# Kernel optimization log

Hardware: AMD Instinct MI355X
Metric: run time of the kernel (lower is better)

Reference implementation:

```python
import jax, jax.numpy as jnp
import numpy as np

EMBED_SIZE = 768
HEAD_SIZE = 64
B, T = 4, 2048


def setup_inputs() -> dict:
    key = jax.random.key(0)
    kx, kk, kq, kv = jax.random.split(key, 4)
    x = jax.random.normal(kx, (B, T, EMBED_SIZE), dtype=jnp.float32)
    # torch Linear(E, H, bias=False): weight [H, E]; stored here as [E, H] for x @ W
    s = 1.0 / np.sqrt(EMBED_SIZE)
    Wk = jax.random.uniform(kk, (EMBED_SIZE, HEAD_SIZE), jnp.float32, -s, s)
    Wq = jax.random.uniform(kq, (EMBED_SIZE, HEAD_SIZE), jnp.float32, -s, s)
    Wv = jax.random.uniform(kv, (EMBED_SIZE, HEAD_SIZE), jnp.float32, -s, s)
    return {"x": x, "Wk": Wk, "Wq": Wq, "Wv": Wv}


def reference(x, Wk, Wq, Wv):
    Bx, Tx, E = x.shape
    k = x @ Wk  # [B, T, H]
    q = x @ Wq
    v = x @ Wv
    w = jnp.einsum("bth,bsh->bts", q, k)  # [B, T, T]
    causal = jnp.tril(jnp.ones((Tx, Tx), dtype=bool))
    # Faithful to source: mask to -inf FIRST, then scale by sqrt(embed_size)
    w = jnp.where(causal, w, -jnp.inf)
    w = w / jnp.sqrt(jnp.asarray(E, dtype=x.dtype))
    w = jax.nn.softmax(w, axis=-1)
    # dropout: eval mode / identity for the correctness baseline
    return jnp.einsum("bts,bsh->bth", w, v)
```

## Files before the change

### kernel.cpp

```cpp
#include <hip/hip_runtime.h>
#include <hip/hip_bf16.h>


typedef __attribute__((ext_vector_type(8))) short short8;
typedef __attribute__((ext_vector_type(4))) float f32x4;

#define SPLIT_KB 4
#define MAX_SP 8

__device__ __forceinline__ unsigned short f2bf(float f) {
    union { float f; unsigned u; } v; v.f = f;
    unsigned r = v.u + 0x7fffu + ((v.u >> 16) & 1u);
    return (unsigned short)(r >> 16);
}

__global__ __launch_bounds__(256) void proj_kernel(const float* __restrict__ x,
                                                   const float* __restrict__ Wk,
                                                   const float* __restrict__ Wq,
                                                   const float* __restrict__ Wv,
                                                   unsigned short* __restrict__ qws,
                                                   unsigned short* __restrict__ kws,
                                                   unsigned short* __restrict__ vT) {
    __shared__ unsigned short xs[32 * 72];
    __shared__ unsigned short wsm[64 * 72];
    const float CSCALE = 1.4426950408889634f / 27.712812921102035f;
    int tid = threadIdx.x;
    int lane = tid & 63, wave = tid >> 6;
    int quad = lane >> 4, l16 = lane & 15;
    int row0 = blockIdx.x * 32;
    int my = blockIdx.y;
    const float* W = (my == 0) ? Wq : (my == 1) ? Wk : Wv;

    int xrow = tid >> 3, xcb = (tid & 7) * 8;
    int wn = tid & 63, wk0 = (tid >> 6) * 16;

    f32x4 acc[2];
    acc[0] = (f32x4)(0.f); acc[1] = (f32x4)(0.f);

    for (int kc = 0; kc < 12; ++kc) {
        __syncthreads();
        {
            const float* src = x + (size_t)(row0 + xrow) * 768 + kc * 64 + xcb;
            float4 f0 = *(const float4*)(src);
            float4 f1 = *(const float4*)(src + 4);
            short8 pk;
            pk[0] = (short)f2bf(f0.x); pk[1] = (short)f2bf(f0.y);
            pk[2] = (short)f2bf(f0.z); pk[3] = (short)f2bf(f0.w);
            pk[4] = (short)f2bf(f1.x); pk[5] = (short)f2bf(f1.y);
            pk[6] = (short)f2bf(f1.z); pk[7] = (short)f2bf(f1.w);
            *(short8*)&xs[xrow * 72 + xcb] = pk;
        }
        {
            float wv[16];
            for (int i = 0; i < 16; ++i)
                wv[i] = W[(size_t)(kc * 64 + wk0 + i) * 64 + wn];
            if (my == 0)
                for (int i = 0; i < 16; ++i) wv[i] *= CSCALE;
            short8 p0, p1;
            for (int i = 0; i < 8; ++i) { p0[i] = (short)f2bf(wv[i]); p1[i] = (short)f2bf(wv[8 + i]); }
            *(short8*)&wsm[wn * 72 + wk0] = p0;
            *(short8*)&wsm[wn * 72 + wk0 + 8] = p1;
        }
        __syncthreads();
        for (int kh = 0; kh < 2; ++kh) {
            int kk = kh * 32 + quad * 8;
            short8 bfr = *(const short8*)&wsm[(wave * 16 + l16) * 72 + kk];
            for (int mt = 0; mt < 2; ++mt) {
                short8 a = *(const short8*)&xs[(mt * 16 + l16) * 72 + kk];
                acc[mt] = __builtin_amdgcn_mfma_f32_16x16x32_bf16(a, bfr, acc[mt], 0, 0, 0);
            }
        }
    }
    __syncthreads();
    int n = wave * 16 + l16;
    if (my != 2) {
        unsigned short* dst = (my == 0) ? qws : kws;
        for (int mt = 0; mt < 2; ++mt)
            for (int j = 0; j < 4; ++j) {
                int rloc = mt * 16 + quad * 4 + j;
                dst[(size_t)(row0 + rloc) * 64 + n] = f2bf(acc[mt][j]);
            }
    } else {
        for (int mt = 0; mt < 2; ++mt)
            for (int j = 0; j < 4; ++j) {
                int rloc = mt * 16 + quad * 4 + j;
                wsm[n * 40 + rloc] = f2bf(acc[mt][j]);
            }
        __syncthreads();
        int bidx = row0 >> 11, t0 = row0 & 2047;
        int c = tid >> 2, rb = (tid & 3) * 8;
        *(short8*)&vT[((size_t)(bidx * 64 + c)) * 2048 + t0 + rb] =
            *(const short8*)&wsm[c * 40 + rb];
    }
}

__global__ __launch_bounds__(64) void attn_split(const unsigned short* __restrict__ qws,
                                                 const unsigned short* __restrict__ kws,
                                                 const unsigned short* __restrict__ vT,
                                                 float* __restrict__ po,
                                                 float* __restrict__ pm,
                                                 float* __restrict__ pl,
                                                 float* __restrict__ out) {
    int bx = blockIdx.x, b = blockIdx.y, sp = blockIdx.z;
    int kbmax = (bx >> 2) + 1;
    int nsp = (kbmax + SPLIT_KB - 1) / SPLIT_KB;
    if (sp >= nsp) return;
    int kb_lo = sp * SPLIT_KB;
    int kb_hi = min(kb_lo + SPLIT_KB, kbmax);

    __shared__ unsigned short ps[16 * 72];
    int lane = threadIdx.x & 63;
    int quad = lane >> 4, l16 = lane & 15;
    int q0 = bx * 16;

    const unsigned short* qp = qws + ((size_t)b * 2048 + q0 + l16) * 64 + quad * 8;
    short8 aq0 = *(const short8*)(qp);
    short8 aq1 = *(const short8*)(qp + 32);

    f32x4 o_acc[4];
    for (int nt = 0; nt < 4; ++nt) o_acc[nt] = (f32x4)(0.f);
    float m_run[4], l_run[4];
    int row_g[4];
    for (int j = 0; j < 4; ++j) {
        m_run[j] = -1e30f; l_run[j] = 0.f;
        row_g[j] = q0 + quad * 4 + j;
    }

    for (int kb = kb_lo; kb < kb_hi; ++kb) {
        const unsigned short* kp =
            kws + ((size_t)b * 2048 + kb * 64 + l16) * 64 + quad * 8;
        f32x4 s[4];
        for (int nt = 0; nt < 4; ++nt) s[nt] = (f32x4)(0.f);
        for (int nt = 0; nt < 4; ++nt) {
            short8 bk0 = *(const short8*)(kp + (size_t)nt * 16 * 64);
            short8 bk1 = *(const short8*)(kp + (size_t)nt * 16 * 64 + 32);
            s[nt] = __builtin_amdgcn_mfma_f32_16x16x32_bf16(aq0, bk0, s[nt], 0, 0, 0);
            s[nt] = __builtin_amdgcn_mfma_f32_16x16x32_bf16(aq1, bk1, s[nt], 0, 0, 0);
        }
        if (kb == kbmax - 1) {
            for (int nt = 0; nt < 4; ++nt) {
                int key = kb * 64 + nt * 16 + l16;
                for (int j = 0; j < 4; ++j)
                    if (key > row_g[j]) s[nt][j] = -1e30f;
            }
        }
        float mx[4], al[4], rs[4];
        for (int j = 0; j < 4; ++j)
            mx[j] = fmaxf(fmaxf(s[0][j], s[1][j]), fmaxf(s[2][j], s[3][j]));
        for (int off = 1; off < 16; off <<= 1)
            for (int j = 0; j < 4; ++j)
                mx[j] = fmaxf(mx[j], __shfl_xor(mx[j], off, 16));
        for (int j = 0; j < 4; ++j) {
            float mn = fmaxf(m_run[j], mx[j]);
            al[j] = exp2f(m_run[j] - mn);
            m_run[j] = mn;
            rs[j] = 0.f;
        }
        for (int nt = 0; nt < 4; ++nt)
            for (int j = 0; j < 4; ++j) {
                float p = exp2f(s[nt][j] - m_run[j]);
                rs[j] += p;
                ps[(quad * 4 + j) * 72 + nt * 16 + l16] = f2bf(p);
            }
        for (int off = 1; off < 16; off <<= 1)
            for (int j = 0; j < 4; ++j)
                rs[j] += __shfl_xor(rs[j], off, 16);
        for (int j = 0; j < 4; ++j) l_run[j] = l_run[j] * al[j] + rs[j];
        for (int nt = 0; nt < 4; ++nt)
            for (int j = 0; j < 4; ++j) o_acc[nt][j] *= al[j];
        const unsigned short* vp =
            vT + ((size_t)b * 64 + l16) * 2048 + kb * 64 + quad * 8;
        for (int kh = 0; kh < 2; ++kh) {
            short8 ap = *(const short8*)&ps[l16 * 72 + kh * 32 + quad * 8];
            for (int nt = 0; nt < 4; ++nt) {
                short8 bv = *(const short8*)(vp + (size_t)nt * 16 * 2048 + kh * 32);
                o_acc[nt] = __builtin_amdgcn_mfma_f32_16x16x32_bf16(ap, bv, o_acc[nt], 0, 0, 0);
            }
        }
    }
    if (nsp == 1) {
        for (int nt = 0; nt < 4; ++nt)
            for (int j = 0; j < 4; ++j)
                out[((size_t)b * 2048 + row_g[j]) * 64 + nt * 16 + l16] =
                    o_acc[nt][j] / l_run[j];
        return;
    }
    int sbase = ((b * 128 + bx) * MAX_SP + sp) * 16;
    for (int nt = 0; nt < 4; ++nt)
        for (int j = 0; j < 4; ++j) {
            int r = quad * 4 + j;
            po[(size_t)(sbase + r) * 64 + nt * 16 + l16] = o_acc[nt][j];
        }
    if (l16 == 0) {
        for (int j = 0; j < 4; ++j) {
            int r = quad * 4 + j;
            pm[sbase + r] = m_run[j];
            pl[sbase + r] = l_run[j];
        }
    }
}

__global__ __launch_bounds__(256) void reduce_kernel(const float* __restrict__ po,
                                                     const float* __restrict__ pm,
                                                     const float* __restrict__ pl,
                                                     float* __restrict__ out) {
    int tid = threadIdx.x;
    int lane = tid & 63, wave = tid >> 6;
    int g = blockIdx.x * 4 + wave;
    int b = g >> 11, t = g & 2047;
    int bx = t >> 4, r = t & 15;
    int kbmax = (bx >> 2) + 1;
    int nsp = (kbmax + SPLIT_KB - 1) / SPLIT_KB;
    if (nsp == 1) return;
    int base = ((b * 128 + bx) * MAX_SP) * 16 + r;
    float mstar = -1e30f;
    for (int sp = 0; sp < nsp; ++sp)
        mstar = fmaxf(mstar, pm[base + sp * 16]);
    float acc = 0.f, lsum = 0.f;
    for (int sp = 0; sp < nsp; ++sp) {
        float w = exp2f(pm[base + sp * 16] - mstar);
        acc += w * po[(size_t)(base + sp * 16) * 64 + lane];
        lsum += w * pl[base + sp * 16];
    }
    out[(size_t)g * 64 + lane] = acc / lsum;
}

extern "C" void kernel_launch(void* const* d_in, const int* in_sizes, int n_in,
                              void* d_out, int out_size, void* d_ws, size_t ws_size,
                              hipStream_t stream) {
    const float* x  = (const float*)d_in[0];
    const float* Wk = (const float*)d_in[1];
    const float* Wq = (const float*)d_in[2];
    const float* Wv = (const float*)d_in[3];
    float* out = (float*)d_out;
    char* w = (char*)d_ws;
    unsigned short* qws = (unsigned short*)w;
    unsigned short* kws = (unsigned short*)(w + 1048576);
    unsigned short* vT  = (unsigned short*)(w + 2097152);
    float* po = (float*)(w + 3145728);
    float* pm = (float*)(w + 19922944);
    float* pl = (float*)(w + 20185088);
    proj_kernel<<<dim3(256, 3), 256, 0, stream>>>(x, Wk, Wq, Wv, qws, kws, vT);
    attn_split<<<dim3(128, 4, MAX_SP), 64, 0, stream>>>(qws, kws, vT, po, pm, pl, out);
    reduce_kernel<<<2048, 256, 0, stream>>>(po, pm, pl, out);
}
```

Baseline: 115.7 us.

## Fuse Q/K/V projections into one block per row tile sharing x

The projection kernel now computes Q, K and V for a 32-row tile in a single 512-thread block instead of launching three blocks per tile that each reload and convert the same x rows. Each of 8 waves handles a 16-row by 48-column slice of the concatenated 192-column output. This cuts x global reads and bf16 conversions by a factor of three, at the cost of fewer blocks (256 instead of 768), a larger shared-memory footprint and narrower per-thread x stores.

Result: slower. 120.2 us (+3.9%).

```diff
diff --git a/kernel.cpp b/kernel.cpp
--- a/kernel.cpp
+++ b/kernel.cpp
@@ -14,7 +14,7 @@
     return (unsigned short)(r >> 16);
 }
 
-__global__ __launch_bounds__(256) void proj_kernel(const float* __restrict__ x,
+__global__ __launch_bounds__(512) void proj_kernel(const float* __restrict__ x,
                                                    const float* __restrict__ Wk,
                                                    const float* __restrict__ Wq,
                                                    const float* __restrict__ Wv,
@@ -22,71 +22,65 @@
                                                    unsigned short* __restrict__ kws,
                                                    unsigned short* __restrict__ vT) {
     __shared__ unsigned short xs[32 * 72];
-    __shared__ unsigned short wsm[64 * 72];
+    __shared__ unsigned short wsm[192 * 72];
     const float CSCALE = 1.4426950408889634f / 27.712812921102035f;
     int tid = threadIdx.x;
     int lane = tid & 63, wave = tid >> 6;
     int quad = lane >> 4, l16 = lane & 15;
+    int wm = wave & 1, wn2 = wave >> 1;
     int row0 = blockIdx.x * 32;
-    int my = blockIdx.y;
-    const float* W = (my == 0) ? Wq : (my == 1) ? Wk : Wv;
-
-    int xrow = tid >> 3, xcb = (tid & 7) * 8;
-    int wn = tid & 63, wk0 = (tid >> 6) * 16;
-
-    f32x4 acc[2];
-    acc[0] = (f32x4)(0.f); acc[1] = (f32x4)(0.f);
+
+    int xrow = tid >> 4, xcb = (tid & 15) * 4;
+    int wn = tid & 63, wk0 = (tid >> 6) * 8;
+
+    f32x4 acc[3];
+    for (int nt = 0; nt < 3; ++nt) acc[nt] = (f32x4)(0.f);
 
     for (int kc = 0; kc < 12; ++kc) {
         __syncthreads();
         {
             const float* src = x + (size_t)(row0 + xrow) * 768 + kc * 64 + xcb;
             float4 f0 = *(const float4*)(src);
-            float4 f1 = *(const float4*)(src + 4);
-            short8 pk;
-            pk[0] = (short)f2bf(f0.x); pk[1] = (short)f2bf(f0.y);
-            pk[2] = (short)f2bf(f0.z); pk[3] = (short)f2bf(f0.w);
-            pk[4] = (short)f2bf(f1.x); pk[5] = (short)f2bf(f1.y);
-            pk[6] = (short)f2bf(f1.z); pk[7] = (short)f2bf(f1.w);
-            *(short8*)&xs[xrow * 72 + xcb] = pk;
-        }
-        {
-            float wv[16];
-            for (int i = 0; i < 16; ++i)
+            unsigned short p0 = f2bf(f0.x), p1 = f2bf(f0.y),
+                           p2 = f2bf(f0.z), p3 = f2bf(f0.w);
+            unsigned short* d = &xs[xrow * 72 + xcb];
+            d[0] = p0; d[1] = p1; d[2] = p2; d[3] = p3;
+        }
+        for (int my = 0; my < 3; ++my) {
+            const float* W = (my == 0) ? Wq : (my == 1) ? Wk : Wv;
+            float wv[8];
+            for (int i = 0; i < 8; ++i)
                 wv[i] = W[(size_t)(kc * 64 + wk0 + i) * 64 + wn];
             if (my == 0)
-                for (int i = 0; i < 16; ++i) wv[i] *= CSCALE;
-            short8 p0, p1;
-            for (int i = 0; i < 8; ++i) { p0[i] = (short)f2bf(wv[i]); p1[i] = (short)f2bf(wv[8 + i]); }
-            *(short8*)&wsm[wn * 72 + wk0] = p0;
-            *(short8*)&wsm[wn * 72 + wk0 + 8] = p1;
+                for (int i = 0; i < 8; ++i) wv[i] *= CSCALE;
+            short8 p;
+            for (int i = 0; i < 8; ++i) p[i] = (short)f2bf(wv[i]);
+            *(short8*)&wsm[(my * 64 + wn) * 72 + wk0] = p;
         }
         __syncthreads();
         for (int kh = 0; kh < 2; ++kh) {
             int kk = kh * 32 + quad * 8;
-            short8 bfr = *(const short8*)&wsm[(wave * 16 + l16) * 72 + kk];
-            for (int mt = 0; mt < 2; ++mt) {
-                short8 a = *(const short8*)&xs[(mt * 16 + l16) * 72 + kk];
-                acc[mt] = __builtin_amdgcn_mfma_f32_16x16x32_bf16(a, bfr, acc[mt], 0, 0, 0);
+            short8 a = *(const short8*)&xs[(wm * 16 + l16) * 72 + kk];
+            for (int nt = 0; nt < 3; ++nt) {
+                short8 bfr = *(const short8*)&wsm[(wn2 * 48 + nt * 16 + l16) * 72 + kk];
+                acc[nt] = __builtin_amdgcn_mfma_f32_16x16x32_bf16(a, bfr, acc[nt], 0, 0, 0);
             }
         }
     }
     __syncthreads();
-    int n = wave * 16 + l16;
-    if (my != 2) {
-        unsigned short* dst = (my == 0) ? qws : kws;
-        for (int mt = 0; mt < 2; ++mt)
-            for (int j = 0; j < 4; ++j) {
-                int rloc = mt * 16 + quad * 4 + j;
-                dst[(size_t)(row0 + rloc) * 64 + n] = f2bf(acc[mt][j]);
-            }
-    } else {
-        for (int mt = 0; mt < 2; ++mt)
-            for (int j = 0; j < 4; ++j) {
-                int rloc = mt * 16 + quad * 4 + j;
-                wsm[n * 40 + rloc] = f2bf(acc[mt][j]);
-            }
-        __syncthreads();
+    for (int nt = 0; nt < 3; ++nt) {
+        int n = wn2 * 48 + nt * 16 + l16;
+        int mat = n >> 6, col = n & 63;
+        for (int j = 0; j < 4; ++j) {
+            int rloc = wm * 16 + quad * 4 + j;
+            unsigned short bv = f2bf(acc[nt][j]);
+            if (mat == 0)      qws[(size_t)(row0 + rloc) * 64 + col] = bv;
+            else if (mat == 1) kws[(size_t)(row0 + rloc) * 64 + col] = bv;
+            else               wsm[col * 40 + rloc] = bv;
+        }
+    }
+    __syncthreads();
+    if (tid < 256) {
         int bidx = row0 >> 11, t0 = row0 & 2047;
         int c = tid >> 2, rb = (tid & 3) * 8;
         *(short8*)&vT[((size_t)(bidx * 64 + c)) * 2048 + t0 + rb] =
@@ -240,7 +234,7 @@
     float* po = (float*)(w + 3145728);
     float* pm = (float*)(w + 19922944);
     float* pl = (float*)(w + 20185088);
-    proj_kernel<<<dim3(256, 3), 256, 0, stream>>>(x, Wk, Wq, Wv, qws, kws, vT);
+    proj_kernel<<<256, 512, 0, stream>>>(x, Wk, Wq, Wv, qws, kws, vT);
     attn_split<<<dim3(128, 4, MAX_SP), 64, 0, stream>>>(qws, kws, vT, po, pm, pl, out);
     reduce_kernel<<<2048, 256, 0, stream>>>(po, pm, pl, out);
 }
```
